# Kernel optimization log

Measured on AMD Instinct MI355X. Metric: run time of the kernel, lower is better.

The kernel has to match this reference:

```python
import jax, jax.numpy as jnp
import numpy as np

B, T, F, E, H, D, L = 4096, 20, 32, 128, 2, 64, 3
EPS = 1e-5


def setup_inputs() -> dict:
    key = jax.random.key(0)
    ks = jax.random.split(key, 16)
    n = lambda k, s, sc=0.05: jax.random.normal(k, s, jnp.float32) * sc
    return {
        'tokens': jax.random.randint(ks[0], (B, T), 0, 50000),
        'field_ids': jax.random.randint(ks[1], (B, F - 1), 0, 1000),
        'word_emb': n(ks[2], (50000, 300)),
        'W_tok': n(ks[3], (300, E)),
        'field_tables': n(ks[4], (F - 1, 1000, E), E ** -0.5),
        'Wq': n(ks[5], (L, E, H * D)),
        'Wk': n(ks[6], (L, E, H * D)),
        'Wv': n(ks[7], (L, E, H * D)),
        'Wres': n(ks[8], (L, E, H * D)),
        'ln_g': jnp.ones((L, H * D), jnp.float32),
        'ln_b': jnp.zeros((L, H * D), jnp.float32),
        'dnn_W1': n(ks[9], (F * E, 1024)),
        'bn1_g': jnp.ones((1024,), jnp.float32), 'bn1_b': jnp.zeros((1024,), jnp.float32),
        'bn1_m': jnp.zeros((1024,), jnp.float32), 'bn1_v': jnp.ones((1024,), jnp.float32),
        'dnn_W2': n(ks[10], (1024, 512)),
        'bn2_g': jnp.ones((512,), jnp.float32), 'bn2_b': jnp.zeros((512,), jnp.float32),
        'bn2_m': jnp.zeros((512,), jnp.float32), 'bn2_v': jnp.ones((512,), jnp.float32),
        'dnn_W3': n(ks[11], (512, 128)),
        'dnn_b3': jnp.zeros((128,), jnp.float32),
        'W_last': n(ks[12], (F * H * D + 128, 1)),
        'b_last': jnp.zeros((1,), jnp.float32),
    }


def _layer_norm(o, g, b):
    mu = o.mean(-1, keepdims=True)
    var = o.var(-1, keepdims=True)
    return (o - mu) / jnp.sqrt(var + EPS) * g + b


def reference(tokens, field_ids, word_emb, W_tok, field_tables, Wq, Wk, Wv, Wres,
              ln_g, ln_b, dnn_W1, bn1_g, bn1_b, bn1_m, bn1_v, dnn_W2, bn2_g, bn2_b,
              bn2_m, bn2_v, dnn_W3, dnn_b3, W_last, b_last):
    # EmbeddingBag(mean) over tokens, then linear to emb_length
    tok_e = word_emb[tokens].mean(1) @ W_tok                      # [B, E]
    # per-field one-hot embedding lookup
    fld_e = field_tables[jnp.arange(F - 1)[None, :], field_ids]    # [B, F-1, E]
    emb = jnp.concatenate([tok_e[:, None, :], fld_e], 1)          # [B, F, E]

    x = emb
    for l in range(L):
        # split(num_out,-1)+cat(...,0) == reshape to heads
        q = (x @ Wq[l]).reshape(B, F, H, D)
        k = (x @ Wk[l]).reshape(B, F, H, D)
        v = (x @ Wv[l]).reshape(B, F, H, D)
        w = jax.nn.softmax(jnp.einsum('bqhd,bkhd->bhqk', q, k) / jnp.sqrt(jnp.float32(D)), -1)
        o = jnp.einsum('bhqk,bkhd->bqhd', w, v).reshape(B, F, H * D)
        o = jax.nn.relu(o + x @ Wres[l])
        x = _layer_norm(o, ln_g[l], ln_b[l])

    att = x.reshape(B, F * H * D)

    # DNN branch (eval mode: BN uses running stats, dropout off)
    h = emb.reshape(B, F * E)
    h = jax.nn.relu((h @ dnn_W1 - bn1_m) / jnp.sqrt(bn1_v + EPS) * bn1_g + bn1_b)
    h = jax.nn.relu((h @ dnn_W2 - bn2_m) / jnp.sqrt(bn2_v + EPS) * bn2_g + bn2_b)
    h = h @ dnn_W3 + dnn_b3

    out = jnp.concatenate([att, h], 1) @ W_last + b_last          # [B, 1]
    return jax.nn.sigmoid(out)
```

## Files before the change

### kernel.cpp

```cpp
#include <hip/hip_runtime.h>
#include <hip/hip_bf16.h>
#include <cstdint>

#define B_  4096
#define T_  20
#define F_  32
#define E_  128
#define H_  2
#define D_  64
#define L_  3
#define HD_ 128
#define EPS_ 1e-5f

typedef __bf16 bfv8 __attribute__((ext_vector_type(8)));
typedef __bf16 bfv4 __attribute__((ext_vector_type(4)));
typedef float  f32x4 __attribute__((ext_vector_type(4)));

__device__ __forceinline__ f32x4 mfma16(bfv8 a, bfv8 b, f32x4 c) {
    return __builtin_amdgcn_mfma_f32_16x16x32_bf16(a, b, c, 0, 0, 0);
}

__device__ __forceinline__ void gload16(const __bf16* g, __bf16* l) {
    __builtin_amdgcn_global_load_lds(
        (const __attribute__((address_space(1))) void*)(g),
        (__attribute__((address_space(3))) void*)(l),
        16, 0, 0);
}

__device__ void transpose_pack_body(const float* __restrict__ in,
                                    __bf16* __restrict__ out,
                                    int K, int N, int bx, int by)
{
    __shared__ float t[64][65];
    int k0 = bx * 64, n0 = by * 64;
    int r = threadIdx.x >> 4, c = (threadIdx.x & 15) * 4;
    for (int rr = r; rr < 64; rr += 16) {
        float4 v = *(const float4*)&in[(int64_t)(k0 + rr) * N + n0 + c];
        t[rr][c] = v.x; t[rr][c + 1] = v.y; t[rr][c + 2] = v.z; t[rr][c + 3] = v.w;
    }
    __syncthreads();
    for (int rr = r; rr < 64; rr += 16) {
        bfv4 o;
        o[0] = (__bf16)t[c + 0][rr];
        o[1] = (__bf16)t[c + 1][rr];
        o[2] = (__bf16)t[c + 2][rr];
        o[3] = (__bf16)t[c + 3][rr];
        *(bfv4*)&out[(int64_t)(n0 + rr) * K + k0 + c] = o;
    }
}

__global__ __launch_bounds__(256) void pack_all_kernel(
    const float* __restrict__ Wq, const float* __restrict__ Wk,
    const float* __restrict__ Wv, const float* __restrict__ Wres,
    __bf16* __restrict__ pkw,
    const float* __restrict__ dW1, __bf16* __restrict__ W1t,
    const float* __restrict__ dW2, __bf16* __restrict__ W2t,
    const float* __restrict__ dW3, __bf16* __restrict__ W3t)
{
    int id = blockIdx.x;
    if (id < 96) {
        int mi = id >> 3, tile = id & 7;
        int l = mi >> 2, p = mi & 3;
        const float* Wb = (p == 0 ? Wq : p == 1 ? Wk : p == 2 ? Wv : Wres) + l * 16384;
        int tid = threadIdx.x;
        int ks = tid >> 6, lane = tid & 63;
        int l15 = lane & 15, lgg = lane >> 4;
        const float* src = Wb + (ks * 32 + lgg * 8) * HD_ + tile * 16 + l15;
        __bf16* dst = pkw + (int64_t)mi * 16384 + ((tile * 4 + ks) * 64 + lane) * 8;
        #pragma unroll
        for (int t = 0; t < 8; t++) dst[t] = (__bf16)src[t * HD_];
    } else if (id < 1120) {
        int t = id - 96;
        transpose_pack_body(dW1, W1t, 4096, 1024, t & 63, t >> 6);
    } else if (id < 1248) {
        int t = id - 1120;
        transpose_pack_body(dW2, W2t, 1024, 512, t & 15, t >> 4);
    } else {
        int t = id - 1248;
        transpose_pack_body(dW3, W3t, 512, 128, t & 7, t >> 3);
    }
}

__global__ __launch_bounds__(256) void embed2_kernel(
    const int* __restrict__ tokens, const float* __restrict__ word_emb,
    const float* __restrict__ W_tok,
    const int* __restrict__ field_ids, const float* __restrict__ field_tables,
    __bf16* __restrict__ embbf)
{
    if (blockIdx.x < 2048) {
        __shared__ float m[2][304];
        int half = threadIdx.x >> 7, t7 = threadIdx.x & 127;
        int b = blockIdx.x * 2 + half;
        float a0 = 0.f, a1 = 0.f, a2 = 0.f;
        const int* tb = tokens + b * T_;
        for (int t = 0; t < T_; t++) {
            const float* row = word_emb + (int64_t)tb[t] * 300;
            a0 += row[t7];
            a1 += row[t7 + 128];
            if (t7 < 44) a2 += row[t7 + 256];
        }
        m[half][t7]       = a0 * (1.f / T_);
        m[half][t7 + 128] = a1 * (1.f / T_);
        if (t7 < 44) m[half][t7 + 256] = a2 * (1.f / T_);
        __syncthreads();
        float s = 0.f;
        for (int e = 0; e < 300; e++) s = fmaf(m[half][e], W_tok[e * E_ + t7], s);
        embbf[(int64_t)b * (F_ * E_) + t7] = (__bf16)s;
    } else {
        int64_t base = (int64_t)(blockIdx.x - 2048) * 1024 + threadIdx.x;
        #pragma unroll
        for (int u = 0; u < 4; u++) {
            int64_t idx = base + u * 256;
            int c = (int)(idx & 31);
            int64_t tmp = idx >> 5;
            int f = (int)(tmp % 31);
            int b = (int)(tmp / 31);
            int ident = field_ids[b * 31 + f];
            const float4* src = (const float4*)field_tables;
            float4 val = src[(int64_t)(f * 1000 + ident) * 32 + c];
            bfv4 o;
            o[0] = (__bf16)val.x; o[1] = (__bf16)val.y;
            o[2] = (__bf16)val.z; o[3] = (__bf16)val.w;
            *(bfv4*)&embbf[(int64_t)b * 4096 + (1 + f) * 128 + c * 4] = o;
        }
    }
}

__global__ __launch_bounds__(256) void gemm128_bt_bf16_bn(
    const __bf16* __restrict__ A, const __bf16* __restrict__ Bt,
    __bf16* __restrict__ C, int M, int N, int K,
    const float* __restrict__ gp, const float* __restrict__ bp,
    const float* __restrict__ mp, const float* __restrict__ vp)
{
    __shared__ __bf16 As[128 * 64];
    __shared__ __bf16 Bs[128 * 64];
    const int tid = threadIdx.x;
    const int wid = tid >> 6, lane = tid & 63;
    const int l15 = lane & 15, lg = lane >> 4;
    const int wr = wid >> 1, wc = wid & 1;
    const int bm = blockIdx.x, bn = blockIdx.y;

    const int srow = lane >> 3, sp = lane & 7;
    const __bf16* Ag[4]; const __bf16* Bg[4];
    __bf16* Ad[4]; __bf16* Bd[4];
    #pragma unroll
    for (int ga = 0; ga < 4; ga++) {
        int row = wid * 32 + ga * 8 + srow;
        int slot = sp ^ (row & 7);
        Ag[ga] = A  + (int64_t)(bm * 128 + row) * K + slot * 8;
        Bg[ga] = Bt + (int64_t)(bn * 128 + row) * K + slot * 8;
        Ad[ga] = &As[(wid * 32 + ga * 8) * 64];
        Bd[ga] = &Bs[(wid * 32 + ga * 8) * 64];
    }

    int ar[2][4], br[2][4];
    #pragma unroll
    for (int ks = 0; ks < 2; ks++) {
        #pragma unroll
        for (int mi = 0; mi < 4; mi++) {
            int rowa = wr * 64 + mi * 16 + l15;
            ar[ks][mi] = rowa * 64 + (((ks * 4 + lg) ^ (rowa & 7)) * 8);
            int rowb = wc * 64 + mi * 16 + l15;
            br[ks][mi] = rowb * 64 + (((ks * 4 + lg) ^ (rowb & 7)) * 8);
        }
    }

    f32x4 acc[4][4];
    #pragma unroll
    for (int mi = 0; mi < 4; mi++)
        #pragma unroll
        for (int ni = 0; ni < 4; ni++) acc[mi][ni] = (f32x4){0.f, 0.f, 0.f, 0.f};

    for (int k0 = 0; k0 < K; k0 += 64) {
        #pragma unroll
        for (int ga = 0; ga < 4; ga++) gload16(Ag[ga] + k0, Ad[ga]);
        #pragma unroll
        for (int ga = 0; ga < 4; ga++) gload16(Bg[ga] + k0, Bd[ga]);
        __syncthreads();
        #pragma unroll
        for (int ks = 0; ks < 2; ks++) {
            bfv8 af[4], bf[4];
            #pragma unroll
            for (int mi = 0; mi < 4; mi++) af[mi] = *(const bfv8*)&As[ar[ks][mi]];
            #pragma unroll
            for (int ni = 0; ni < 4; ni++) bf[ni] = *(const bfv8*)&Bs[br[ks][ni]];
            #pragma unroll
            for (int mi = 0; mi < 4; mi++)
                #pragma unroll
                for (int ni = 0; ni < 4; ni++)
                    acc[mi][ni] = mfma16(af[mi], bf[ni], acc[mi][ni]);
        }
        __syncthreads();
    }

    float inv[4], sh[4];
    #pragma unroll
    for (int ni = 0; ni < 4; ni++) {
        int col = bn * 128 + wc * 64 + ni * 16 + l15;
        float iv = rsqrtf(vp[col] + EPS_) * gp[col];
        inv[ni] = iv;
        sh[ni] = bp[col] - mp[col] * iv;
    }
    #pragma unroll
    for (int mi = 0; mi < 4; mi++)
        #pragma unroll
        for (int ni = 0; ni < 4; ni++) {
            int col = bn * 128 + wc * 64 + ni * 16 + l15;
            #pragma unroll
            for (int r = 0; r < 4; r++) {
                int row = bm * 128 + wr * 64 + mi * 16 + lg * 4 + r;
                float y = fmaxf(fmaf(acc[mi][ni][r], inv[ni], sh[ni]), 0.f);
                C[(int64_t)row * N + col] = (__bf16)y;
            }
        }
}

template <int OUTBF, int EPI>
__global__ __launch_bounds__(256) void gemm_bt_bf16(
    const __bf16* __restrict__ A, const __bf16* __restrict__ Bt,
    void* __restrict__ Cout, int M, int N, int K,
    const float* __restrict__ gp, const float* __restrict__ bp,
    const float* __restrict__ mp, const float* __restrict__ vp)
{
    __shared__ __bf16 As[128 * 64];
    __shared__ __bf16 Bs[64 * 64];
    const int tid = threadIdx.x;
    const int wid = tid >> 6, lane = tid & 63;
    const int l15 = lane & 15, lg = lane >> 4;
    const int wr = wid >> 1, wc = wid & 1;
    const int bm = blockIdx.x, bn = blockIdx.y;

    const int srow = lane >> 3, sp = lane & 7;
    const __bf16* Ag[4]; const __bf16* Bg[2];
    __bf16* Ad[4]; __bf16* Bd[2];
    #pragma unroll
    for (int ga = 0; ga < 4; ga++) {
        int row = wid * 32 + ga * 8 + srow;
        int slot = sp ^ (row & 7);
        Ag[ga] = A + (int64_t)(bm * 128 + row) * K + slot * 8;
        Ad[ga] = &As[(wid * 32 + ga * 8) * 64];
    }
    #pragma unroll
    for (int gb = 0; gb < 2; gb++) {
        int row = wid * 16 + gb * 8 + srow;
        int slot = sp ^ (row & 7);
        Bg[gb] = Bt + (int64_t)(bn * 64 + row) * K + slot * 8;
        Bd[gb] = &Bs[(wid * 16 + gb * 8) * 64];
    }

    int ar[2][4], br2[2][2];
    #pragma unroll
    for (int ks = 0; ks < 2; ks++) {
        #pragma unroll
        for (int mi = 0; mi < 4; mi++) {
            int row = wr * 64 + mi * 16 + l15;
            ar[ks][mi] = row * 64 + (((ks * 4 + lg) ^ (row & 7)) * 8);
        }
        #pragma unroll
        for (int ni = 0; ni < 2; ni++) {
            int row = wc * 32 + ni * 16 + l15;
            br2[ks][ni] = row * 64 + (((ks * 4 + lg) ^ (row & 7)) * 8);
        }
    }

    f32x4 acc[4][2];
    #pragma unroll
    for (int mi = 0; mi < 4; mi++)
        #pragma unroll
        for (int ni = 0; ni < 2; ni++) acc[mi][ni] = (f32x4){0.f, 0.f, 0.f, 0.f};

    for (int k0 = 0; k0 < K; k0 += 64) {
        #pragma unroll
        for (int ga = 0; ga < 4; ga++) gload16(Ag[ga] + k0, Ad[ga]);
        #pragma unroll
        for (int gb = 0; gb < 2; gb++) gload16(Bg[gb] + k0, Bd[gb]);
        __syncthreads();
        #pragma unroll
        for (int ks = 0; ks < 2; ks++) {
            bfv8 af[4], bf2[2];
            #pragma unroll
            for (int mi = 0; mi < 4; mi++) af[mi] = *(const bfv8*)&As[ar[ks][mi]];
            #pragma unroll
            for (int ni = 0; ni < 2; ni++) bf2[ni] = *(const bfv8*)&Bs[br2[ks][ni]];
            #pragma unroll
            for (int mi = 0; mi < 4; mi++)
                #pragma unroll
                for (int ni = 0; ni < 2; ni++)
                    acc[mi][ni] = mfma16(af[mi], bf2[ni], acc[mi][ni]);
        }
        __syncthreads();
    }

    float inv[2], sh[2];
    #pragma unroll
    for (int ni = 0; ni < 2; ni++) {
        int col = bn * 64 + wc * 32 + ni * 16 + l15;
        if constexpr (EPI == 0) {
            float iv = rsqrtf(vp[col] + EPS_) * gp[col];
            inv[ni] = iv;
            sh[ni] = bp[col] - mp[col] * iv;
        } else {
            inv[ni] = 1.f;
            sh[ni] = bp[col];
        }
    }
    #pragma unroll
    for (int mi = 0; mi < 4; mi++)
        #pragma unroll
        for (int ni = 0; ni < 2; ni++) {
            int col = bn * 64 + wc * 32 + ni * 16 + l15;
            #pragma unroll
            for (int r = 0; r < 4; r++) {
                int row = bm * 128 + wr * 64 + mi * 16 + lg * 4 + r;
                float y = fmaf(acc[mi][ni][r], inv[ni], sh[ni]);
                if constexpr (EPI == 0) y = fmaxf(y, 0.f);
                if constexpr (OUTBF)
                    ((__bf16*)Cout)[(int64_t)row * N + col] = (__bf16)y;
                else
                    ((float*)Cout)[(int64_t)row * N + col] = y;
            }
        }
}

__global__ __launch_bounds__(512, 4) void attn3_head_kernel(
    const __bf16* __restrict__ embbf, const __bf16* __restrict__ pkw,
    const float* __restrict__ lng, const float* __restrict__ lnb,
    const float* __restrict__ h3, const float* __restrict__ Wl,
    const float* __restrict__ bl, float* __restrict__ out)
{
    __shared__ __bf16 smem[8192 * 4 + 4096];
    __shared__ float  part[2][128];
    __bf16* xs  = smem;
    __bf16* qf  = smem + 8192;
    __bf16* kf  = smem + 16384;
    __bf16* vtf = smem + 24576;
    __bf16* pf  = smem + 32768;

    const int tid = threadIdx.x;
    const int wid = tid >> 6, lane = tid & 63;
    const int l15 = lane & 15, lg = lane >> 4;
    const int arow = wid >> 2, h = (wid >> 1) & 1, qh = wid & 1;
    const int q = qh * 16 + l15;
    const int half = (lg & 1) * 4;

    {
        const __bf16* src = embbf + (int64_t)blockIdx.x * 8192;
        #pragma unroll
        for (int u = 0; u < 2; u++) {
            int g = u * 512 + tid;
            int ln = g & 63;
            int fld = (((g >> 8) & 1) << 4) + (ln & 15);
            int e0 = ((g >> 6) & 3) * 32 + (ln >> 4) * 8;
            int br = g >> 9;
            bfv8 v = *(const bfv8*)&src[br * 4096 + fld * 128 + e0];
            *(bfv8*)&xs[g * 8] = v;
        }
    }
    __syncthreads();

    float head_partial = 0.f;

    for (int l = 0; l < L_; l++) {
        #pragma unroll 1
        for (int cc = 0; cc < 3; cc++) {
            const int col = wid * 3 + cc;
            const int mat = col >> 3, m = col & 7;
            const __bf16* W = pkw + (l * 4 + mat) * 16384;
            bfv8 wf[4];
            #pragma unroll
            for (int ks = 0; ks < 4; ks++)
                wf[ks] = *(const bfv8*)(W + ((m * 4 + ks) * 64 + lane) * 8);
            f32x4 pc[4];
            #pragma unroll
            for (int i = 0; i < 4; i++) pc[i] = (f32x4){0.f, 0.f, 0.f, 0.f};

            if (mat == 2) {
                #pragma unroll
                for (int i = 0; i < 4; i++) {
                    int gbase = ((i >> 1) * 8 + (i & 1) * 4) * 64;
                    #pragma unroll
                    for (int ks = 0; ks < 4; ks++) {
                        bfv8 xv = *(const bfv8*)&xs[(gbase + ks * 64 + lane) * 8];
                        pc[i] = mfma16(xv, wf[ks], pc[i]);
                    }
                }
            } else {
                #pragma unroll
                for (int i = 0; i < 4; i++) {
                    int gbase = ((i >> 1) * 8 + (i & 1) * 4) * 64;
                    #pragma unroll
                    for (int ks = 0; ks < 4; ks++) {
                        bfv8 xv = *(const bfv8*)&xs[(gbase + ks * 64 + lane) * 8];
                        pc[i] = mfma16(wf[ks], xv, pc[i]);
                    }
                }
            }

            if (mat == 0) {
                const int ln2 = ((((m << 1) + (lg >> 1)) & 3) << 4) + l15;
                #pragma unroll
                for (int i = 0; i < 4; i++) {
                    bfv4 v4;
                    #pragma unroll
                    for (int r = 0; r < 4; r++) v4[r] = (__bf16)(pc[i][r] * 0.125f);
                    int g = ((i >> 1) * 8 + (i & 1) * 4 + (m >> 1)) * 64 + ln2;
                    *(bfv4*)&qf[g * 8 + half] = v4;
                }
            } else if (mat == 1) {
                const int ln2 = ((((m << 1) + (lg >> 1)) & 3) << 4) + l15;
                #pragma unroll
                for (int i = 0; i < 4; i++) {
                    bfv4 v4;
                    #pragma unroll
                    for (int r = 0; r < 4; r++) v4[r] = (__bf16)pc[i][r];
                    int g = ((i >> 1) * 8 + (i & 1) * 4 + (m >> 1)) * 64 + ln2;
                    *(bfv4*)&kf[g * 8 + half] = v4;
                }
            } else {
                #pragma unroll
                for (int i = 0; i < 4; i++) {
                    bfv4 v4;
                    #pragma unroll
                    for (int r = 0; r < 4; r++) v4[r] = (__bf16)pc[i][r];
                    int lnv = ((((i & 1) * 2 + (lg >> 1)) & 3) << 4) + l15;
                    int g = ((i >> 1) * 8 + m) * 64 + lnv;
                    *(bfv4*)&vtf[g * 8 + half] = v4;
                }
            }
        }
        __syncthreads();

        const __bf16* Wr = pkw + (l * 4 + 3) * 16384;
        bfv8 wr0[4], wr1[4], wr2[4], wr3[4];
        #pragma unroll
        for (int ks = 0; ks < 4; ks++) {
            wr0[ks] = *(const bfv8*)(Wr + (((h * 4 + 0) * 4 + ks) * 64 + lane) * 8);
            wr1[ks] = *(const bfv8*)(Wr + (((h * 4 + 1) * 4 + ks) * 64 + lane) * 8);
            wr2[ks] = *(const bfv8*)(Wr + (((h * 4 + 2) * 4 + ks) * 64 + lane) * 8);
            wr3[ks] = *(const bfv8*)(Wr + (((h * 4 + 3) * 4 + ks) * 64 + lane) * 8);
        }

        f32x4 sc2[2] = {(f32x4){0.f, 0.f, 0.f, 0.f}, (f32x4){0.f, 0.f, 0.f, 0.f}};
        #pragma unroll
        for (int ksp = 0; ksp < 2; ksp++) {
            int dks = h * 2 + ksp;
            bfv8 qb = *(const bfv8*)&qf[((arow * 8 + qh * 4 + dks) * 64 + lane) * 8];
            #pragma unroll
            for (int km = 0; km < 2; km++) {
                bfv8 kb = *(const bfv8*)&kf[((arow * 8 + km * 4 + dks) * 64 + lane) * 8];
                sc2[km] = mfma16(kb, qb, sc2[km]);
            }
        }

        f32x4 macc[4];
        {
            bfv8 xr[4];
            #pragma unroll
            for (int ks = 0; ks < 4; ks++)
                xr[ks] = *(const bfv8*)&xs[((arow * 8 + qh * 4 + ks) * 64 + lane) * 8];
            macc[0] = (f32x4){0.f, 0.f, 0.f, 0.f};
            macc[1] = (f32x4){0.f, 0.f, 0.f, 0.f};
            macc[2] = (f32x4){0.f, 0.f, 0.f, 0.f};
            macc[3] = (f32x4){0.f, 0.f, 0.f, 0.f};
            #pragma unroll
            for (int ks = 0; ks < 4; ks++) {
                macc[0] = mfma16(wr0[ks], xr[ks], macc[0]);
                macc[1] = mfma16(wr1[ks], xr[ks], macc[1]);
                macc[2] = mfma16(wr2[ks], xr[ks], macc[2]);
                macc[3] = mfma16(wr3[ks], xr[ks], macc[3]);
            }
        }

        float mx = -1e30f;
        #pragma unroll
        for (int km = 0; km < 2; km++)
            #pragma unroll
            for (int r = 0; r < 4; r++) mx = fmaxf(mx, sc2[km][r]);
        mx = fmaxf(mx, __shfl_xor(mx, 16));
        mx = fmaxf(mx, __shfl_xor(mx, 32));
        float pv[2][4];
        float sum = 0.f;
        #pragma unroll
        for (int km = 0; km < 2; km++)
            #pragma unroll
            for (int r = 0; r < 4; r++) {
                float e = __expf(sc2[km][r] - mx);
                pv[km][r] = e; sum += e;
            }
        sum += __shfl_xor(sum, 16);
        sum += __shfl_xor(sum, 32);
        float inv = 1.f / sum;

        __bf16* pw = pf + wid * 512;
        #pragma unroll
        for (int km = 0; km < 2; km++) {
            int ln2 = (((km * 2 + (lg >> 1)) & 3) << 4) + l15;
            bfv4 v4;
            #pragma unroll
            for (int r = 0; r < 4; r++) v4[r] = (__bf16)(pv[km][r] * inv);
            *(bfv4*)&pw[ln2 * 8 + half] = v4;
        }
        bfv8 pb = *(const bfv8*)&pw[lane * 8];
        #pragma unroll
        for (int dm = 0; dm < 4; dm++) {
            bfv8 va = *(const bfv8*)&vtf[((arow * 8 + h * 4 + dm) * 64 + lane) * 8];
            macc[dm] = mfma16(va, pb, macc[dm]);
        }

        float yv[4][4];
        float s1 = 0.f, s2 = 0.f;
        #pragma unroll
        for (int dm = 0; dm < 4; dm++) {
            #pragma unroll
            for (int r = 0; r < 4; r++) {
                float v = fmaxf(macc[dm][r], 0.f);
                yv[dm][r] = v;
                s1 += v; s2 += v * v;
            }
        }
        s1 += __shfl_xor(s1, 16); s1 += __shfl_xor(s1, 32);
        s2 += __shfl_xor(s2, 16); s2 += __shfl_xor(s2, 32);
        if (lg == 0) { part[arow][q * 4 + h * 2] = s1; part[arow][q * 4 + h * 2 + 1] = s2; }
        __syncthreads();

        f32x4 pt = *(const f32x4*)&part[arow][q * 4];
        float mean = (pt[0] + pt[2]) * (1.f / 128.f);
        float var  = (pt[1] + pt[3]) * (1.f / 128.f) - mean * mean;
        float rstd = rsqrtf(var + EPS_);
        const float* lgp = lng + l * HD_;
        const float* lbp = lnb + l * HD_;

        if (l < L_ - 1) {
            #pragma unroll
            for (int dm = 0; dm < 4; dm++) {
                int j = h * 64 + dm * 16 + lg * 4;
                float4 g  = *(const float4*)(lgp + j);
                float4 bb = *(const float4*)(lbp + j);
                bfv4 y;
                y[0] = (__bf16)((yv[dm][0] - mean) * rstd * g.x + bb.x);
                y[1] = (__bf16)((yv[dm][1] - mean) * rstd * g.y + bb.y);
                y[2] = (__bf16)((yv[dm][2] - mean) * rstd * g.z + bb.z);
                y[3] = (__bf16)((yv[dm][3] - mean) * rstd * g.w + bb.w);
                int ks2 = h * 2 + (dm >> 1);
                int ln2 = (((dm * 2 + (lg >> 1)) & 3) << 4) + l15;
                int g2 = (arow * 8 + qh * 4 + ks2) * 64 + ln2;
                *(bfv4*)&xs[g2 * 8 + half] = y;
            }
            __syncthreads();
        } else {
            #pragma unroll
            for (int dm = 0; dm < 4; dm++) {
                int j = h * 64 + dm * 16 + lg * 4;
                float4 g  = *(const float4*)(lgp + j);
                float4 bb = *(const float4*)(lbp + j);
                float4 w  = *(const float4*)(Wl + q * HD_ + j);
                head_partial = fmaf((yv[dm][0] - mean) * rstd * g.x + bb.x, w.x, head_partial);
                head_partial = fmaf((yv[dm][1] - mean) * rstd * g.y + bb.y, w.y, head_partial);
                head_partial = fmaf((yv[dm][2] - mean) * rstd * g.z + bb.z, w.z, head_partial);
                head_partial = fmaf((yv[dm][3] - mean) * rstd * g.w + bb.w, w.w, head_partial);
            }
        }
    }

    float* red = (float*)pf;
    red[tid] = head_partial;
    __syncthreads();
    if ((wid & 3) == 0) {
        int br = wid >> 2;
        int base = br * 256;
        float s = red[base + lane] + red[base + 64 + lane]
                + red[base + 128 + lane] + red[base + 192 + lane];
        int64_t b0 = (int64_t)blockIdx.x * 2 + br;
        s += h3[b0 * 128 + lane]      * Wl[4096 + lane];
        s += h3[b0 * 128 + 64 + lane] * Wl[4096 + 64 + lane];
        #pragma unroll
        for (int off = 32; off; off >>= 1) s += __shfl_down(s, off);
        if (lane == 0) out[b0] = 1.f / (1.f + __expf(-(s + bl[0])));
    }
}

extern "C" void kernel_launch(void* const* d_in, const int* in_sizes, int n_in,
                              void* d_out, int out_size, void* d_ws, size_t ws_size,
                              hipStream_t stream)
{
    const int*   tokens       = (const int*)  d_in[0];
    const int*   field_ids    = (const int*)  d_in[1];
    const float* word_emb     = (const float*)d_in[2];
    const float* W_tok        = (const float*)d_in[3];
    const float* field_tables = (const float*)d_in[4];
    const float* Wq           = (const float*)d_in[5];
    const float* Wk           = (const float*)d_in[6];
    const float* Wv           = (const float*)d_in[7];
    const float* Wres         = (const float*)d_in[8];
    const float* ln_g         = (const float*)d_in[9];
    const float* ln_b         = (const float*)d_in[10];
    const float* dnn_W1       = (const float*)d_in[11];
    const float* bn1_g        = (const float*)d_in[12];
    const float* bn1_b        = (const float*)d_in[13];
    const float* bn1_m        = (const float*)d_in[14];
    const float* bn1_v        = (const float*)d_in[15];
    const float* dnn_W2       = (const float*)d_in[16];
    const float* bn2_g        = (const float*)d_in[17];
    const float* bn2_b        = (const float*)d_in[18];
    const float* bn2_m        = (const float*)d_in[19];
    const float* bn2_v        = (const float*)d_in[20];
    const float* dnn_W3       = (const float*)d_in[21];
    const float* dnn_b3       = (const float*)d_in[22];
    const float* W_last       = (const float*)d_in[23];
    const float* b_last       = (const float*)d_in[24];
    float* out = (float*)d_out;

    const int64_t embN = (int64_t)B_ * F_ * E_;
    __bf16* embbf = (__bf16*)d_ws;
    float*  h3    = (float*)(embbf + embN);
    __bf16* pkw   = (__bf16*)(h3 + (int64_t)B_ * 128);
    __bf16* W1t   = pkw + 12 * 16384;
    __bf16* W2t   = W1t + (int64_t)1024 * 4096;
    __bf16* W3t   = W2t + (int64_t)512 * 1024;
    __bf16* h1bf  = W3t + (int64_t)128 * 512;
    __bf16* h2bf  = h1bf + (int64_t)B_ * 1024;

    pack_all_kernel<<<1264, 256, 0, stream>>>(
        Wq, Wk, Wv, Wres, pkw, dnn_W1, W1t, dnn_W2, W2t, dnn_W3, W3t);

    embed2_kernel<<<6016, 256, 0, stream>>>(
        tokens, word_emb, W_tok, field_ids, field_tables, embbf);

    gemm128_bt_bf16_bn<<<dim3(32, 8), 256, 0, stream>>>(
        embbf, W1t, h1bf, B_, 1024, 4096, bn1_g, bn1_b, bn1_m, bn1_v);
    gemm_bt_bf16<1, 0><<<dim3(32, 8), 256, 0, stream>>>(
        h1bf, W2t, h2bf, B_, 512, 1024, bn2_g, bn2_b, bn2_m, bn2_v);
    gemm_bt_bf16<0, 1><<<dim3(32, 2), 256, 0, stream>>>(
        h2bf, W3t, h3, B_, 128, 512, nullptr, dnn_b3, nullptr, nullptr);

    attn3_head_kernel<<<B_ / 2, 512, 0, stream>>>(
        embbf, pkw, ln_g, ln_b, h3, W_last, b_last, out);
}
```

Baseline: 240.0 us.

## Co-schedule W1 GEMM and attention in one launch, add combine kernel

Merges the large DNN first-layer GEMM (rewritten for 512-thread blocks with a 4x2 wave layout) and the attention stack into a single heterogeneous kernel. The first 256 blocks do the GEMM and the rest do attention, so the two independent branches can run on the GPU at the same time instead of back to back. The attention blocks now write partial logits to a buffer. A new small combine kernel adds the DNN head term and applies the sigmoid after the remaining GEMMs. The trade-offs are an extra launch, an extra workspace buffer, and a GEMM block shape that may run less efficiently.

```diff
diff --git a/kernel.cpp b/kernel.cpp
--- a/kernel.cpp
+++ b/kernel.cpp
@@ -126,95 +126,6 @@
     }
 }
 
-__global__ __launch_bounds__(256) void gemm128_bt_bf16_bn(
-    const __bf16* __restrict__ A, const __bf16* __restrict__ Bt,
-    __bf16* __restrict__ C, int M, int N, int K,
-    const float* __restrict__ gp, const float* __restrict__ bp,
-    const float* __restrict__ mp, const float* __restrict__ vp)
-{
-    __shared__ __bf16 As[128 * 64];
-    __shared__ __bf16 Bs[128 * 64];
-    const int tid = threadIdx.x;
-    const int wid = tid >> 6, lane = tid & 63;
-    const int l15 = lane & 15, lg = lane >> 4;
-    const int wr = wid >> 1, wc = wid & 1;
-    const int bm = blockIdx.x, bn = blockIdx.y;
-
-    const int srow = lane >> 3, sp = lane & 7;
-    const __bf16* Ag[4]; const __bf16* Bg[4];
-    __bf16* Ad[4]; __bf16* Bd[4];
-    #pragma unroll
-    for (int ga = 0; ga < 4; ga++) {
-        int row = wid * 32 + ga * 8 + srow;
-        int slot = sp ^ (row & 7);
-        Ag[ga] = A  + (int64_t)(bm * 128 + row) * K + slot * 8;
-        Bg[ga] = Bt + (int64_t)(bn * 128 + row) * K + slot * 8;
-        Ad[ga] = &As[(wid * 32 + ga * 8) * 64];
-        Bd[ga] = &Bs[(wid * 32 + ga * 8) * 64];
-    }
-
-    int ar[2][4], br[2][4];
-    #pragma unroll
-    for (int ks = 0; ks < 2; ks++) {
-        #pragma unroll
-        for (int mi = 0; mi < 4; mi++) {
-            int rowa = wr * 64 + mi * 16 + l15;
-            ar[ks][mi] = rowa * 64 + (((ks * 4 + lg) ^ (rowa & 7)) * 8);
-            int rowb = wc * 64 + mi * 16 + l15;
-            br[ks][mi] = rowb * 64 + (((ks * 4 + lg) ^ (rowb & 7)) * 8);
-        }
-    }
-
-    f32x4 acc[4][4];
-    #pragma unroll
-    for (int mi = 0; mi < 4; mi++)
-        #pragma unroll
-        for (int ni = 0; ni < 4; ni++) acc[mi][ni] = (f32x4){0.f, 0.f, 0.f, 0.f};
-
-    for (int k0 = 0; k0 < K; k0 += 64) {
-        #pragma unroll
-        for (int ga = 0; ga < 4; ga++) gload16(Ag[ga] + k0, Ad[ga]);
-        #pragma unroll
-        for (int ga = 0; ga < 4; ga++) gload16(Bg[ga] + k0, Bd[ga]);
-        __syncthreads();
-        #pragma unroll
-        for (int ks = 0; ks < 2; ks++) {
-            bfv8 af[4], bf[4];
-            #pragma unroll
-            for (int mi = 0; mi < 4; mi++) af[mi] = *(const bfv8*)&As[ar[ks][mi]];
-            #pragma unroll
-            for (int ni = 0; ni < 4; ni++) bf[ni] = *(const bfv8*)&Bs[br[ks][ni]];
-            #pragma unroll
-            for (int mi = 0; mi < 4; mi++)
-                #pragma unroll
-                for (int ni = 0; ni < 4; ni++)
-                    acc[mi][ni] = mfma16(af[mi], bf[ni], acc[mi][ni]);
-        }
-        __syncthreads();
-    }
-
-    float inv[4], sh[4];
-    #pragma unroll
-    for (int ni = 0; ni < 4; ni++) {
-        int col = bn * 128 + wc * 64 + ni * 16 + l15;
-        float iv = rsqrtf(vp[col] + EPS_) * gp[col];
-        inv[ni] = iv;
-        sh[ni] = bp[col] - mp[col] * iv;
-    }
-    #pragma unroll
-    for (int mi = 0; mi < 4; mi++)
-        #pragma unroll
-        for (int ni = 0; ni < 4; ni++) {
-            int col = bn * 128 + wc * 64 + ni * 16 + l15;
-            #pragma unroll
-            for (int r = 0; r < 4; r++) {
-                int row = bm * 128 + wr * 64 + mi * 16 + lg * 4 + r;
-                float y = fmaxf(fmaf(acc[mi][ni][r], inv[ni], sh[ni]), 0.f);
-                C[(int64_t)row * N + col] = (__bf16)y;
-            }
-        }
-}
-
 template <int OUTBF, int EPI>
 __global__ __launch_bounds__(256) void gemm_bt_bf16(
     const __bf16* __restrict__ A, const __bf16* __restrict__ Bt,
@@ -322,29 +233,124 @@
         }
 }
 
-__global__ __launch_bounds__(512, 4) void attn3_head_kernel(
-    const __bf16* __restrict__ embbf, const __bf16* __restrict__ pkw,
+#define W1_BLOCKS_ 256
+
+__global__ __launch_bounds__(512, 4) void mega_w1_attn_kernel(
+    const __bf16* __restrict__ embbf, const __bf16* __restrict__ W1t,
+    __bf16* __restrict__ h1bf,
+    const float* __restrict__ bn1g, const float* __restrict__ bn1b,
+    const float* __restrict__ bn1m, const float* __restrict__ bn1v,
+    const __bf16* __restrict__ pkw,
     const float* __restrict__ lng, const float* __restrict__ lnb,
-    const float* __restrict__ h3, const float* __restrict__ Wl,
-    const float* __restrict__ bl, float* __restrict__ out)
+    const float* __restrict__ Wl, float* __restrict__ attnp)
 {
     __shared__ __bf16 smem[8192 * 4 + 4096];
     __shared__ float  part[2][128];
+
+    const int tid = threadIdx.x;
+    const int wid = tid >> 6, lane = tid & 63;
+    const int l15 = lane & 15, lg = lane >> 4;
+
+    if (blockIdx.x < W1_BLOCKS_) {
+        __bf16* As = smem;
+        __bf16* Bs = smem + 8192;
+        const int wr = wid >> 2, wc = wid & 3;
+        const int bm = blockIdx.x >> 3, bn = blockIdx.x & 7;
+        const int K = 4096, N = 1024;
+
+        const int srow = lane >> 3, sp = lane & 7;
+        const __bf16* Ag[2]; const __bf16* Bg[2];
+        __bf16* Ad[2]; __bf16* Bd[2];
+        #pragma unroll
+        for (int c = 0; c < 2; c++) {
+            int rbase = wid * 16 + c * 8;
+            int row = rbase + srow;
+            int slot = sp ^ (row & 7);
+            Ag[c] = embbf + (int64_t)(bm * 128 + row) * K + slot * 8;
+            Bg[c] = W1t   + (int64_t)(bn * 128 + row) * K + slot * 8;
+            Ad[c] = &As[rbase * 64];
+            Bd[c] = &Bs[rbase * 64];
+        }
+
+        int ar[2][4], br[2][2];
+        #pragma unroll
+        for (int ks = 0; ks < 2; ks++) {
+            #pragma unroll
+            for (int mi = 0; mi < 4; mi++) {
+                int rowa = wr * 64 + mi * 16 + l15;
+                ar[ks][mi] = rowa * 64 + (((ks * 4 + lg) ^ (rowa & 7)) * 8);
+            }
+            #pragma unroll
+            for (int ni = 0; ni < 2; ni++) {
+                int rowb = wc * 32 + ni * 16 + l15;
+                br[ks][ni] = rowb * 64 + (((ks * 4 + lg) ^ (rowb & 7)) * 8);
+            }
+        }
+
+        f32x4 acc[4][2];
+        #pragma unroll
+        for (int mi = 0; mi < 4; mi++)
+            #pragma unroll
+            for (int ni = 0; ni < 2; ni++) acc[mi][ni] = (f32x4){0.f, 0.f, 0.f, 0.f};
+
+        for (int k0 = 0; k0 < K; k0 += 64) {
+            #pragma unroll
+            for (int c = 0; c < 2; c++) gload16(Ag[c] + k0, Ad[c]);
+            #pragma unroll
+            for (int c = 0; c < 2; c++) gload16(Bg[c] + k0, Bd[c]);
+            __syncthreads();
+            #pragma unroll
+            for (int ks = 0; ks < 2; ks++) {
+                bfv8 af[4], bf[2];
+                #pragma unroll
+                for (int mi = 0; mi < 4; mi++) af[mi] = *(const bfv8*)&As[ar[ks][mi]];
+                #pragma unroll
+                for (int ni = 0; ni < 2; ni++) bf[ni] = *(const bfv8*)&Bs[br[ks][ni]];
+                #pragma unroll
+                for (int mi = 0; mi < 4; mi++)
+                    #pragma unroll
+                    for (int ni = 0; ni < 2; ni++)
+                        acc[mi][ni] = mfma16(af[mi], bf[ni], acc[mi][ni]);
+            }
+            __syncthreads();
+        }
+
+        float inv[2], sh[2];
+        #pragma unroll
+        for (int ni = 0; ni < 2; ni++) {
+            int col = bn * 128 + wc * 32 + ni * 16 + l15;
+            float iv = rsqrtf(bn1v[col] + EPS_) * bn1g[col];
+            inv[ni] = iv;
+            sh[ni] = bn1b[col] - bn1m[col] * iv;
+        }
+        #pragma unroll
+        for (int mi = 0; mi < 4; mi++)
+            #pragma unroll
+            for (int ni = 0; ni < 2; ni++) {
+                int col = bn * 128 + wc * 32 + ni * 16 + l15;
+                #pragma unroll
+                for (int r = 0; r < 4; r++) {
+                    int row = bm * 128 + wr * 64 + mi * 16 + lg * 4 + r;
+                    float y = fmaxf(fmaf(acc[mi][ni][r], inv[ni], sh[ni]), 0.f);
+                    h1bf[(int64_t)row * N + col] = (__bf16)y;
+                }
+            }
+        return;
+    }
+
+    const int ablk = blockIdx.x - W1_BLOCKS_;
     __bf16* xs  = smem;
     __bf16* qf  = smem + 8192;
     __bf16* kf  = smem + 16384;
     __bf16* vtf = smem + 24576;
     __bf16* pf  = smem + 32768;
 
-    const int tid = threadIdx.x;
-    const int wid = tid >> 6, lane = tid & 63;
-    const int l15 = lane & 15, lg = lane >> 4;
     const int arow = wid >> 2, h = (wid >> 1) & 1, qh = wid & 1;
     const int q = qh * 16 + l15;
     const int half = (lg & 1) * 4;
 
     {
-        const __bf16* src = embbf + (int64_t)blockIdx.x * 8192;
+        const __bf16* src = embbf + (int64_t)ablk * 8192;
         #pragma unroll
         for (int u = 0; u < 2; u++) {
             int g = u * 512 + tid;
@@ -570,13 +576,24 @@
         int base = br * 256;
         float s = red[base + lane] + red[base + 64 + lane]
                 + red[base + 128 + lane] + red[base + 192 + lane];
-        int64_t b0 = (int64_t)blockIdx.x * 2 + br;
-        s += h3[b0 * 128 + lane]      * Wl[4096 + lane];
-        s += h3[b0 * 128 + 64 + lane] * Wl[4096 + 64 + lane];
         #pragma unroll
         for (int off = 32; off; off >>= 1) s += __shfl_down(s, off);
-        if (lane == 0) out[b0] = 1.f / (1.f + __expf(-(s + bl[0])));
-    }
+        if (lane == 0) attnp[(int64_t)ablk * 2 + br] = s;
+    }
+}
+
+__global__ __launch_bounds__(256) void combine_kernel(
+    const float* __restrict__ attnp, const float* __restrict__ h3,
+    const float* __restrict__ Wl, const float* __restrict__ bl,
+    float* __restrict__ out)
+{
+    int b = blockIdx.x * 4 + (threadIdx.x >> 6);
+    int lane = threadIdx.x & 63;
+    float s = h3[(int64_t)b * 128 + lane]      * Wl[4096 + lane]
+            + h3[(int64_t)b * 128 + 64 + lane] * Wl[4096 + 64 + lane];
+    #pragma unroll
+    for (int off = 32; off; off >>= 1) s += __shfl_down(s, off);
+    if (lane == 0) out[b] = 1.f / (1.f + __expf(-(s + attnp[b] + bl[0])));
 }
 
 extern "C" void kernel_launch(void* const* d_in, const int* in_sizes, int n_in,
@@ -619,6 +636,7 @@
     __bf16* W3t   = W2t + (int64_t)512 * 1024;
     __bf16* h1bf  = W3t + (int64_t)128 * 512;
     __bf16* h2bf  = h1bf + (int64_t)B_ * 1024;
+    float*  attnp = (float*)(h2bf + (int64_t)B_ * 512);
 
     pack_all_kernel<<<1264, 256, 0, stream>>>(
         Wq, Wk, Wv, Wres, pkw, dnn_W1, W1t, dnn_W2, W2t, dnn_W3, W3t);
@@ -626,13 +644,14 @@
     embed2_kernel<<<6016, 256, 0, stream>>>(
         tokens, word_emb, W_tok, field_ids, field_tables, embbf);
 
-    gemm128_bt_bf16_bn<<<dim3(32, 8), 256, 0, stream>>>(
-        embbf, W1t, h1bf, B_, 1024, 4096, bn1_g, bn1_b, bn1_m, bn1_v);
+    mega_w1_attn_kernel<<<W1_BLOCKS_ + B_ / 2, 512, 0, stream>>>(
+        embbf, W1t, h1bf, bn1_g, bn1_b, bn1_m, bn1_v,
+        pkw, ln_g, ln_b, W_last, attnp);
+
     gemm_bt_bf16<1, 0><<<dim3(32, 8), 256, 0, stream>>>(
         h1bf, W2t, h2bf, B_, 512, 1024, bn2_g, bn2_b, bn2_m, bn2_v);
     gemm_bt_bf16<0, 1><<<dim3(32, 2), 256, 0, stream>>>(
         h2bf, W3t, h3, B_, 128, 512, nullptr, dnn_b3, nullptr, nullptr);
 
-    attn3_head_kernel<<<B_ / 2, 512, 0, stream>>>(
-        embbf, pkw, ln_g, ln_b, h3, W_last, b_last, out);
-}
+    combine_kernel<<<B_ / 4, 256, 0, stream>>>(attnp, h3, W_last, b_last, out);
+}
```

Result: faster. 205.5 us (-14.4%).
